# Performance work log

Hardware: AMD Instinct MI355X
Metric: run time of the kernel (lower is better)

Reference implementation:

```python
import jax, jax.numpy as jnp
import numpy as np

LAYERS, UNITS, B, T = 3, 1024, 128, 256


def setup_inputs() -> dict:
    key = jax.random.key(0)
    k1, k2, k3, k4, k5 = jax.random.split(key, 5)
    scale = 0.03  # keep gate pre-activations in a sane range
    return {
        "input_seq": jax.random.normal(k1, (B, T, UNITS), dtype=jnp.float32),
        "initial_states": jax.random.normal(k2, (B, UNITS, LAYERS), dtype=jnp.float32),
        "W": jax.random.normal(k3, (LAYERS, UNITS, 3 * UNITS), dtype=jnp.float32) * scale,
        "U": jax.random.normal(k4, (LAYERS, UNITS, 3 * UNITS), dtype=jnp.float32) * scale,
        "b": jax.random.normal(k5, (LAYERS, 2, 3 * UNITS), dtype=jnp.float32) * scale,
    }


def _gru_layer(x, h0, Wl, Ul, bl):
    """Keras GRU (reset_after=True), inference mode. x: [B,T,F], h0: [B,U]."""
    u = h0.shape[-1]
    # Precompute input projections for all timesteps: [B,T,3U] -> scan over T.
    xw = jnp.einsum("btf,fg->btg", x, Wl) + bl[0]
    xw_t = jnp.swapaxes(xw, 0, 1)  # [T,B,3U]

    def step(h, xw_step):
        hu = h @ Ul + bl[1]  # [B,3U]
        xz, xr, xh = xw_step[:, :u], xw_step[:, u:2 * u], xw_step[:, 2 * u:]
        hz, hr, hh = hu[:, :u], hu[:, u:2 * u], hu[:, 2 * u:]
        z = jax.nn.sigmoid(xz + hz)
        r = jax.nn.sigmoid(xr + hr)
        hhat = jnp.tanh(xh + r * hh)
        h_new = z * h + (1.0 - z) * hhat
        return h_new, h_new

    h_last, ys = jax.lax.scan(step, h0, xw_t)
    return jnp.swapaxes(ys, 0, 1), h_last  # [B,T,U], [B,U]


def reference(input_seq, initial_states, W, U, b):
    x = input_seq
    states = []
    for i in range(LAYERS):
        x, h = _gru_layer(x, initial_states[:, :, i], W[i], U[i], b[i])
        states.append(h)
    return x, jnp.stack(states, axis=-1)  # [B,T,U], [B,U,L]
```

## Files before the change

### kernel.cpp

```cpp
#include <hip/hip_runtime.h>
#include <cstdint>
#include <cstddef>


#define UNITS 1024
#define U3 3072
#define BATCH 128
#define TSTEPS 256

typedef _Float16 h16;
typedef __attribute__((ext_vector_type(8))) _Float16 h16x8;
typedef __attribute__((ext_vector_type(4))) _Float16 h16x4;
typedef __attribute__((ext_vector_type(4))) float f32x4;
typedef __attribute__((ext_vector_type(4))) unsigned int u32x4;

#define GAS __attribute__((address_space(1)))
#define LAS __attribute__((address_space(3)))
#define ASYNC16(g, l) __builtin_amdgcn_global_load_lds((const GAS unsigned int*)(g), (LAS unsigned int*)(l), 16, 0, 0)

__device__ __forceinline__ float sigmf(float x) { return 1.0f / (1.0f + __expf(-x)); }
__device__ __forceinline__ float tanhf_fast(float x) { return 2.0f / (1.0f + __expf(-2.0f * x)) - 1.0f; }

__global__ void k_cvt_x(const float* __restrict__ x, h16* __restrict__ xo) {
  const int m = blockIdx.x;
  const int t = m >> 7, b = m & 127;
  const int u = threadIdx.x << 2;
  const float4 v = *(const float4*)(x + (size_t)((b << 8) + t) * UNITS + u);
  h16x4 o; o[0] = (h16)v.x; o[1] = (h16)v.y; o[2] = (h16)v.z; o[3] = (h16)v.w;
  *(h16x4*)(xo + (size_t)m * UNITS + u) = o;
}

__global__ void k_trans(const float* __restrict__ src, h16* __restrict__ dst) {
  __shared__ float sT[32][33];
  const int l = blockIdx.z;
  const int n0 = blockIdx.x << 5, k0 = blockIdx.y << 5;
  const int tx = threadIdx.x, ty = threadIdx.y;
  const float* s = src + (size_t)l * UNITS * U3;
  h16* d = dst + (size_t)l * U3 * UNITS;
#pragma unroll
  for (int r = 0; r < 4; ++r)
    sT[ty + r * 8][tx] = s[(size_t)(k0 + ty + r * 8) * U3 + n0 + tx];
  __syncthreads();
#pragma unroll
  for (int r = 0; r < 4; ++r)
    d[(size_t)(n0 + ty + r * 8) * UNITS + k0 + tx] = (h16)sT[tx][ty + r * 8];
}

__global__ void k_cvt_h(const float* __restrict__ init, h16* __restrict__ h0) {
  const int idx = blockIdx.x * 256 + threadIdx.x;
  const int l = idx >> 17, r = idx & 131071;
  h0[idx] = (h16)init[(size_t)r * 3 + l];
}

__global__ void k_zero(int* __restrict__ p, int n) {
  const int i = blockIdx.x * 256 + threadIdx.x;
  if (i < n) p[i] = 0;
}

__global__ __launch_bounds__(256) void k_gemm_xw(
    const h16* __restrict__ A, const h16* __restrict__ Bt,
    const float* __restrict__ bias, h16* __restrict__ C) {
  __shared__ __align__(16) h16 sA[128 * 32];
  __shared__ __align__(16) h16 sB[128 * 32];
  const int tid = threadIdx.x;
  const int lane = tid & 63, wave = tid >> 6;
  const int wm = (wave & 1) << 6, wn = (wave >> 1) << 6;
  const int m0 = blockIdx.x << 7;
  const int n0 = blockIdx.y << 7;
  const int crow = tid >> 2, ck = (tid & 3) << 3;
  const int fm = lane & 15, fq = lane >> 4;
  f32x4 acc[4][4] = {};
  for (int k0 = 0; k0 < 1024; k0 += 32) {
    ASYNC16(A + (size_t)(m0 + crow) * 1024 + k0 + ck,      sA + wave * 512);
    ASYNC16(A + (size_t)(m0 + 64 + crow) * 1024 + k0 + ck, sA + 2048 + wave * 512);
    ASYNC16(Bt + (size_t)(n0 + crow) * 1024 + k0 + ck,      sB + wave * 512);
    ASYNC16(Bt + (size_t)(n0 + 64 + crow) * 1024 + k0 + ck, sB + 2048 + wave * 512);
    __syncthreads();
    h16x8 af[4], bfv[4];
#pragma unroll
    for (int i = 0; i < 4; ++i)
      af[i] = *(const h16x8*)(sA + (wm + i * 16 + fm) * 32 + fq * 8);
#pragma unroll
    for (int j = 0; j < 4; ++j)
      bfv[j] = *(const h16x8*)(sB + (wn + j * 16 + fm) * 32 + fq * 8);
#pragma unroll
    for (int i = 0; i < 4; ++i)
#pragma unroll
      for (int j = 0; j < 4; ++j)
        acc[i][j] = __builtin_amdgcn_mfma_f32_16x16x32_f16(af[i], bfv[j], acc[i][j], 0, 0, 0);
    __syncthreads();
  }
#pragma unroll
  for (int j = 0; j < 4; ++j) {
    const int col = n0 + wn + j * 16 + fm;
    const float bv = bias[col];
#pragma unroll
    for (int i = 0; i < 4; ++i) {
      const int row = m0 + wm + i * 16 + fq * 4;
#pragma unroll
      for (int r = 0; r < 4; ++r)
        C[(size_t)(row + r) * U3 + col] = (h16)(acc[i][j][r] + bv);
    }
  }
}

__global__ __launch_bounds__(128) void k_rec(
    const h16* __restrict__ Ut,
    const float* __restrict__ b1,
    const h16* __restrict__ xw,
    const h16* __restrict__ h0l,
    h16* __restrict__ P0,
    h16* __restrict__ P1,
    h16* __restrict__ y16,
    float* __restrict__ yf,
    float* __restrict__ st,
    int* __restrict__ flags,
    const int l) {
  __shared__ __align__(16) h16 sU[49152];
  const int tid = threadIdx.x;
  const int lane = tid & 63, w = tid >> 6;
  const int b = blockIdx.x;
  const int c = b & 63, rg = b >> 6;
  const int c0 = c << 4;
  const int fm = lane & 15, fq = lane >> 4;

#pragma unroll
  for (int kk = 0; kk < 32; ++kk) {
#pragma unroll
    for (int g = 0; g < 3; ++g) {
      const int i = kk * 3 + g;
      if ((i & 1) == w)
        ASYNC16(Ut + (size_t)((g << 10) + c0 + fm) * 1024 + (kk << 5) + (fq << 3),
                sU + (size_t)i * 512);
    }
  }
  const int col = c0 + fm;
  const float bz = b1[col], br = b1[1024 + col], bh = b1[2048 + col];
  const int r0 = (rg << 5) + (w << 4);
  const int rowA = r0 + fm;
  const int rQ = r0 + (fq << 2);
  const int* fpoll = flags + (rg << 6) + lane;
  int* fpost = flags + (rg << 6) + c;
  __syncthreads();

  for (int t = 0; t < TSTEPS; ++t) {
    if (t > 0) {
      const int target = (l << 8) + t;
      int f;
      do {
        asm volatile("global_load_dword %0, %1, off sc0 sc1\n\ts_waitcnt vmcnt(0)"
                     : "=v"(f) : "v"(fpoll) : "memory");
      } while (!__all(f >= target));
    }
    const h16* hin = (t == 0) ? h0l : ((t & 1) ? P0 : P1);
    h16* hout = (t & 1) ? P1 : P0;

    u32x4 raw[32];
    const h16* Ab = hin + (size_t)rowA * 1024 + (fq << 3);
#pragma unroll
    for (int kk = 0; kk < 32; ++kk)
      asm volatile("global_load_dwordx4 %0, %1, off offset:%2 sc0 sc1"
                   : "=v"(raw[kk]) : "v"(Ab), "n"(kk * 64));
    unsigned int hpu[4];
    const h16* hqa = hin + (size_t)rQ * 1024 + col;
    const h16* hqb = hqa + 2048;
    asm volatile("global_load_ushort %0, %1, off sc0 sc1"             : "=v"(hpu[0]) : "v"(hqa));
    asm volatile("global_load_ushort %0, %1, off offset:2048 sc0 sc1" : "=v"(hpu[1]) : "v"(hqa));
    asm volatile("global_load_ushort %0, %1, off sc0 sc1"             : "=v"(hpu[2]) : "v"(hqb));
    asm volatile("global_load_ushort %0, %1, off offset:2048 sc0 sc1" : "=v"(hpu[3]) : "v"(hqb));

    const h16* xq = xw + (size_t)(t * 128 + rQ) * U3 + col;
    float px[4], pr[4], ph[4];
#pragma unroll
    for (int r = 0; r < 4; ++r) {
      px[r] = (float)xq[(size_t)r * U3];
      pr[r] = (float)xq[(size_t)r * U3 + 1024];
      ph[r] = (float)xq[(size_t)r * U3 + 2048];
    }
    asm volatile("s_waitcnt vmcnt(0)" ::: "memory");
    __builtin_amdgcn_sched_barrier(0);

    f32x4 a0 = {}, a1 = {}, a2 = {};
#pragma unroll
    for (int kk = 0; kk < 32; ++kk) {
      union { u32x4 u; h16x8 h; } ac; ac.u = raw[kk];
      const h16* bb = sU + (size_t)(kk * 3) * 512 + (lane << 3);
      const h16x8 vz = *(const h16x8*)(bb);
      const h16x8 vr = *(const h16x8*)(bb + 512);
      const h16x8 vh = *(const h16x8*)(bb + 1024);
      a0 = __builtin_amdgcn_mfma_f32_16x16x32_f16(ac.h, vz, a0, 0, 0, 0);
      a1 = __builtin_amdgcn_mfma_f32_16x16x32_f16(ac.h, vr, a1, 0, 0, 0);
      a2 = __builtin_amdgcn_mfma_f32_16x16x32_f16(ac.h, vh, a2, 0, 0, 0);
    }

    h16* so = hout + (size_t)rQ * 1024 + col;
#pragma unroll
    for (int r = 0; r < 4; ++r) {
      union { unsigned short s; h16 h; } cv; cv.s = (unsigned short)hpu[r];
      const float hp = (float)cv.h;
      const float z   = sigmf(px[r] + a0[r] + bz);
      const float rgt = sigmf(pr[r] + a1[r] + br);
      const float hh  = tanhf_fast(ph[r] + rgt * (a2[r] + bh));
      const float hn  = z * hp + (1.0f - z) * hh;
      union { unsigned short s; h16 h; } ov; ov.h = (h16)hn;
      const unsigned int ob = ov.s;
      if (r == 0) asm volatile("global_store_short %0, %1, off sc0 sc1"             :: "v"(so), "v"(ob) : "memory");
      if (r == 1) asm volatile("global_store_short %0, %1, off offset:2048 sc0 sc1" :: "v"(so), "v"(ob) : "memory");
      if (r == 2) asm volatile("global_store_short %0, %1, off sc0 sc1"             :: "v"(so + 2048), "v"(ob) : "memory");
      if (r == 3) asm volatile("global_store_short %0, %1, off offset:2048 sc0 sc1" :: "v"(so + 2048), "v"(ob) : "memory");
      const int row = rQ + r;
      if (y16) y16[(size_t)(t * 128 + row) * 1024 + col] = (h16)hn;
      if (yf)  yf[(size_t)(row * 256 + t) * 1024 + col] = hn;
      if (t == 255) st[(size_t)(row * 1024 + col) * 3] = hn;
    }
    __syncthreads();
    if (tid == 0) {
      const int fv = (l << 8) + t + 1;
      asm volatile("global_store_dword %0, %1, off sc0 sc1" :: "v"(fpost), "v"(fv) : "memory");
    }
  }
}

extern "C" void kernel_launch(void* const* d_in, const int* in_sizes, int n_in,
                              void* d_out, int out_size, void* d_ws, size_t ws_size,
                              hipStream_t stream) {
  const float* x_in  = (const float*)d_in[0];
  const float* h0_in = (const float*)d_in[1];
  const float* W     = (const float*)d_in[2];
  const float* U     = (const float*)d_in[3];
  const float* bias  = (const float*)d_in[4];
  float* out = (float*)d_out;

  char* ws = (char*)d_ws;
  h16* x16 = (h16*)(ws);
  h16* xw  = (h16*)(ws + 67108864);
  h16* Wt  = (h16*)(ws + 268435456);
  h16* Ut  = (h16*)(ws + 287309824);
  h16* h0b = (h16*)(ws + 306184192);
  h16* P0  = (h16*)(ws + 306970624);

  h16* P1A    = (h16*)((char*)d_out + 134217728 - 262144);
  int* flagsA = (int*)((char*)d_out + 134217728 - 262144 - 16384);
  h16* P1B    = (h16*)ws;
  int* flags2 = (int*)(ws + 262144);

  k_cvt_x<<<TSTEPS * BATCH, 256, 0, stream>>>(x_in, x16);
  k_trans<<<dim3(96, 32, 3), dim3(32, 8), 0, stream>>>(W, Wt);
  k_trans<<<dim3(96, 32, 3), dim3(32, 8), 0, stream>>>(U, Ut);
  k_cvt_h<<<1536, 256, 0, stream>>>(h0_in, h0b);
  k_zero<<<16, 256, 0, stream>>>(flagsA, 4096);

  for (int l = 0; l < 3; ++l) {
    const float* b0 = bias + (size_t)l * 6144;
    const float* b1 = bias + (size_t)l * 6144 + 3072;
    k_gemm_xw<<<dim3(256, 24), 256, 0, stream>>>(x16, Wt + (size_t)l * U3 * UNITS, b0, xw);
    if (l == 2) k_zero<<<16, 256, 0, stream>>>(flags2, 4096);
    h16* P1    = (l < 2) ? P1A : P1B;
    int* flags = (l < 2) ? flagsA : flags2;
    h16* y16p  = (l < 2) ? x16 : nullptr;
    float* yfp = (l == 2) ? out : nullptr;
    float* stp = out + 33554432 + l;
    k_rec<<<256, 128, 0, stream>>>(Ut + (size_t)l * U3 * UNITS, b1, xw,
                                   h0b + (size_t)l * BATCH * UNITS,
                                   P0, P1, y16p, yfp, stp, flags, l);
  }
}
```

Measured before the change: 7.324 ms.

## Use per-wave flags, split MFMA wait, and defer output stores past flag post

Each wave now posts its own progress flag right after its hidden-state stores drain, which removes the block-wide __syncthreads before signalling. Pollers read four flags per lane with a dwordx4 load. The xw gate inputs are loaded with inline asm after the h loads, so the first half of the MFMA chain can start once the first 16 A-fragments arrive (vmcnt(32)) instead of waiting for every load. The y16/yf/state output stores move after the flag post to shorten the critical path between steps. The flag array doubles in size and correctness now rests on the hand-written vmcnt counts.

```diff
diff --git a/kernel.cpp b/kernel.cpp
--- a/kernel.cpp
+++ b/kernel.cpp
@@ -104,7 +104,7 @@
   }
 }
 
-__global__ __launch_bounds__(128) void k_rec(
+__global__ __launch_bounds__(128, 1) void k_rec(
     const h16* __restrict__ Ut,
     const float* __restrict__ b1,
     const h16* __restrict__ xw,
@@ -139,18 +139,19 @@
   const int r0 = (rg << 5) + (w << 4);
   const int rowA = r0 + fm;
   const int rQ = r0 + (fq << 2);
-  const int* fpoll = flags + (rg << 6) + lane;
-  int* fpost = flags + (rg << 6) + c;
+  const int* fpoll = flags + (rg << 7) + ((lane & 31) << 2);
+  int* fpost = flags + (rg << 7) + (c << 1) + w;
   __syncthreads();
 
   for (int t = 0; t < TSTEPS; ++t) {
     if (t > 0) {
       const int target = (l << 8) + t;
-      int f;
+      u32x4 f;
       do {
-        asm volatile("global_load_dword %0, %1, off sc0 sc1\n\ts_waitcnt vmcnt(0)"
+        asm volatile("global_load_dwordx4 %0, %1, off sc0 sc1\n\ts_waitcnt vmcnt(0)"
                      : "=v"(f) : "v"(fpoll) : "memory");
-      } while (!__all(f >= target));
+      } while (!__all((int)f[0] >= target && (int)f[1] >= target &&
+                      (int)f[2] >= target && (int)f[3] >= target));
     }
     const h16* hin = (t == 0) ? h0l : ((t & 1) ? P0 : P1);
     h16* hout = (t & 1) ? P1 : P0;
@@ -168,55 +169,71 @@
     asm volatile("global_load_ushort %0, %1, off offset:2048 sc0 sc1" : "=v"(hpu[1]) : "v"(hqa));
     asm volatile("global_load_ushort %0, %1, off sc0 sc1"             : "=v"(hpu[2]) : "v"(hqb));
     asm volatile("global_load_ushort %0, %1, off offset:2048 sc0 sc1" : "=v"(hpu[3]) : "v"(hqb));
-
-    const h16* xq = xw + (size_t)(t * 128 + rQ) * U3 + col;
-    float px[4], pr[4], ph[4];
-#pragma unroll
-    for (int r = 0; r < 4; ++r) {
-      px[r] = (float)xq[(size_t)r * U3];
-      pr[r] = (float)xq[(size_t)r * U3 + 1024];
-      ph[r] = (float)xq[(size_t)r * U3 + 2048];
+    unsigned int xwb[12];
+    {
+      const h16* xq = xw + (size_t)(t * 128 + rQ) * U3 + col;
+#pragma unroll
+      for (int r = 0; r < 4; ++r) {
+        const h16* xa = xq + (size_t)r * U3;
+        const h16* xb2 = xa + 2048;
+        asm volatile("global_load_ushort %0, %1, off"             : "=v"(xwb[r * 3 + 0]) : "v"(xa));
+        asm volatile("global_load_ushort %0, %1, off offset:2048" : "=v"(xwb[r * 3 + 1]) : "v"(xa));
+        asm volatile("global_load_ushort %0, %1, off"             : "=v"(xwb[r * 3 + 2]) : "v"(xb2));
+      }
+    }
+
+    f32x4 a0 = {}, a1 = {}, a2 = {};
+#pragma unroll
+    for (int half = 0; half < 2; ++half) {
+      if (half == 0) asm volatile("s_waitcnt vmcnt(32)" ::: "memory");
+      else           asm volatile("s_waitcnt vmcnt(16)" ::: "memory");
+      __builtin_amdgcn_sched_barrier(0);
+#pragma unroll
+      for (int kk = half * 16; kk < half * 16 + 16; ++kk) {
+        union { u32x4 u; h16x8 h; } ac; ac.u = raw[kk];
+        const h16* bb = sU + (size_t)(kk * 3) * 512 + (lane << 3);
+        const h16x8 vz = *(const h16x8*)(bb);
+        const h16x8 vr = *(const h16x8*)(bb + 512);
+        const h16x8 vh = *(const h16x8*)(bb + 1024);
+        a0 = __builtin_amdgcn_mfma_f32_16x16x32_f16(ac.h, vz, a0, 0, 0, 0);
+        a1 = __builtin_amdgcn_mfma_f32_16x16x32_f16(ac.h, vr, a1, 0, 0, 0);
+        a2 = __builtin_amdgcn_mfma_f32_16x16x32_f16(ac.h, vh, a2, 0, 0, 0);
+      }
     }
     asm volatile("s_waitcnt vmcnt(0)" ::: "memory");
     __builtin_amdgcn_sched_barrier(0);
 
-    f32x4 a0 = {}, a1 = {}, a2 = {};
-#pragma unroll
-    for (int kk = 0; kk < 32; ++kk) {
-      union { u32x4 u; h16x8 h; } ac; ac.u = raw[kk];
-      const h16* bb = sU + (size_t)(kk * 3) * 512 + (lane << 3);
-      const h16x8 vz = *(const h16x8*)(bb);
-      const h16x8 vr = *(const h16x8*)(bb + 512);
-      const h16x8 vh = *(const h16x8*)(bb + 1024);
-      a0 = __builtin_amdgcn_mfma_f32_16x16x32_f16(ac.h, vz, a0, 0, 0, 0);
-      a1 = __builtin_amdgcn_mfma_f32_16x16x32_f16(ac.h, vr, a1, 0, 0, 0);
-      a2 = __builtin_amdgcn_mfma_f32_16x16x32_f16(ac.h, vh, a2, 0, 0, 0);
-    }
-
     h16* so = hout + (size_t)rQ * 1024 + col;
+    float hn[4];
 #pragma unroll
     for (int r = 0; r < 4; ++r) {
-      union { unsigned short s; h16 h; } cv; cv.s = (unsigned short)hpu[r];
-      const float hp = (float)cv.h;
-      const float z   = sigmf(px[r] + a0[r] + bz);
-      const float rgt = sigmf(pr[r] + a1[r] + br);
-      const float hh  = tanhf_fast(ph[r] + rgt * (a2[r] + bh));
-      const float hn  = z * hp + (1.0f - z) * hh;
-      union { unsigned short s; h16 h; } ov; ov.h = (h16)hn;
+      union { unsigned short s; h16 h; } cv;
+      cv.s = (unsigned short)hpu[r];       const float hp = (float)cv.h;
+      cv.s = (unsigned short)xwb[r * 3 + 0]; const float xz = (float)cv.h;
+      cv.s = (unsigned short)xwb[r * 3 + 1]; const float xr = (float)cv.h;
+      cv.s = (unsigned short)xwb[r * 3 + 2]; const float xh = (float)cv.h;
+      const float z   = sigmf(xz + a0[r] + bz);
+      const float rgt = sigmf(xr + a1[r] + br);
+      const float hh  = tanhf_fast(xh + rgt * (a2[r] + bh));
+      hn[r] = z * hp + (1.0f - z) * hh;
+      union { unsigned short s; h16 h; } ov; ov.h = (h16)hn[r];
       const unsigned int ob = ov.s;
       if (r == 0) asm volatile("global_store_short %0, %1, off sc0 sc1"             :: "v"(so), "v"(ob) : "memory");
       if (r == 1) asm volatile("global_store_short %0, %1, off offset:2048 sc0 sc1" :: "v"(so), "v"(ob) : "memory");
       if (r == 2) asm volatile("global_store_short %0, %1, off sc0 sc1"             :: "v"(so + 2048), "v"(ob) : "memory");
       if (r == 3) asm volatile("global_store_short %0, %1, off offset:2048 sc0 sc1" :: "v"(so + 2048), "v"(ob) : "memory");
-      const int row = rQ + r;
-      if (y16) y16[(size_t)(t * 128 + row) * 1024 + col] = (h16)hn;
-      if (yf)  yf[(size_t)(row * 256 + t) * 1024 + col] = hn;
-      if (t == 255) st[(size_t)(row * 1024 + col) * 3] = hn;
-    }
-    __syncthreads();
-    if (tid == 0) {
+    }
+    asm volatile("s_waitcnt vmcnt(0)" ::: "memory");
+    if (lane == 0) {
       const int fv = (l << 8) + t + 1;
       asm volatile("global_store_dword %0, %1, off sc0 sc1" :: "v"(fpost), "v"(fv) : "memory");
+    }
+#pragma unroll
+    for (int r = 0; r < 4; ++r) {
+      const int row = rQ + r;
+      if (y16) y16[(size_t)(t * 128 + row) * 1024 + col] = (h16)hn[r];
+      if (yf)  yf[(size_t)(row * 256 + t) * 1024 + col] = hn[r];
+      if (t == 255) st[(size_t)(row * 1024 + col) * 3] = hn[r];
     }
   }
 }
```

Result: faster. 5.994 ms (-18.2%).
